# Optimization experiments

Hardware: AMD Instinct MI355X
Metric: run time of the kernel (lower is better)

Reference implementation:

```python
import jax, jax.numpy as jnp
import numpy as np
import math

B, N, D, K = 128, 2048, 256, 64


def setup_inputs() -> dict:
    key = jax.random.key(0)
    ks = jax.random.split(key, 8)
    latent = jax.random.normal(ks[0], (B, N, D), dtype=jnp.float32)
    token_mask = jax.random.uniform(ks[1], (B, N)) < 0.7
    token_mask = token_mask.at[:, 0].set(True)  # guarantee >=1 valid token per row
    scale = 1.0 / math.sqrt(D)
    Wq = jax.random.normal(ks[2], (D, D), dtype=jnp.float32) * scale
    bq = jax.random.normal(ks[3], (D,), dtype=jnp.float32) * 0.01
    Wk = jax.random.normal(ks[4], (D, D), dtype=jnp.float32) * scale
    bk = jax.random.normal(ks[5], (D,), dtype=jnp.float32) * 0.01
    Ws = jax.random.normal(ks[6], (D,), dtype=jnp.float32) * scale
    bs = jax.random.normal(ks[7], (1,), dtype=jnp.float32) * 0.01
    return {"latent": latent, "token_mask": token_mask, "Wq": Wq, "bq": bq,
            "Wk": Wk, "bk": bk, "Ws": Ws, "bs": bs}


def reference(latent, token_mask, Wq, bq, Wk, bk, Ws, bs):
    # latent: [B, N, D], token_mask: [B, N] bool
    d = latent.shape[-1]
    ego = latent[:, :1, :]                                   # [B, 1, D]
    query = jnp.einsum('bod,ed->boe', ego, Wq) + bq          # [B, 1, D]
    keys = jnp.einsum('bnd,ed->bne', latent, Wk) + bk        # [B, N, D]
    similarity = jnp.sum(query * keys, axis=-1) / jnp.sqrt(jnp.float32(d))  # [B, N]
    saliency = jnp.einsum('bnd,d->bn', latent, Ws) + bs[0]   # [B, N]
    scores = similarity + saliency
    scores = jnp.where(token_mask, scores, -jnp.inf)
    # force_ego = False -> no inf injection at slot 0
    selected_scores, selected_indices = jax.lax.top_k(scores, K)  # [B, K]
    # batched_index_select along token dim
    selected_tokens = jnp.take_along_axis(latent, selected_indices[:, :, None], axis=1)  # [B, K, D]
    sel_mask_f = jnp.take_along_axis(token_mask.astype(jnp.float32)[:, :, None],
                                     selected_indices[:, :, None], axis=1)[:, :, 0]
    selected_mask = sel_mask_f > 0.5                          # [B, K]
    # masked mean over token dim
    m = token_mask.astype(latent.dtype)
    global_latent = jnp.einsum('bnd,bn->bd', latent, m) / jnp.sum(m, axis=1, keepdims=True)  # [B, D]
    importance = jax.nn.softmax(jnp.where(selected_mask, selected_scores, -1e9), axis=1)     # [B, K]
    return selected_tokens, selected_mask, selected_indices, importance, global_latent
```

## Files before the change

### kernel.cpp

```cpp
#include <hip/hip_runtime.h>
#include <math.h>

#define B 128
#define N 2048
#define D 256
#define K 64
#define CH 16
#define RPC (N / CH)
#define MASKED_KEY 0x007FFFFFu

typedef unsigned long long u64;

#define OFF_V       0
#define OFF_C2      (OFF_V + B * D)
#define OFF_CNT     (OFF_C2 + B)
#define OFF_PART    (OFF_CNT + B)
#define OFF_MODE    (OFF_PART + B * CH * D)
#define OFF_LISTS   (OFF_MODE + 64)

#define O_TOK   0
#define O_MASK  (O_TOK + B * K * D)
#define O_IDX   (O_MASK + B * K)
#define O_IMP   (O_IDX + B * K)
#define O_GLOB  (O_IMP + B * K)

__device__ __forceinline__ bool mask_at(const void* p, int mode, int i) {
    if (mode == 1) return ((const unsigned char*)p)[i] != 0;
    if (mode == 2) return ((const float*)p)[i] != 0.0f;
    return ((const int*)p)[i] != 0;
}

__device__ __forceinline__ u64 wave_sort_desc(u64 P, int l) {
    #pragma unroll
    for (int k2 = 2; k2 <= 64; k2 <<= 1) {
        #pragma unroll
        for (int j = k2 >> 1; j >= 1; j >>= 1) {
            u64 o = __shfl_xor(P, j, 64);
            bool lower = (l & j) == 0;
            bool descB = (l & k2) == 0;
            bool og = o > P;
            if (og == (lower == descB)) P = o;
        }
    }
    return P;
}

__device__ __forceinline__ u64 wave_merge_desc(u64 P, int l) {
    #pragma unroll
    for (int j = 32; j >= 1; j >>= 1) {
        u64 o = __shfl_xor(P, j, 64);
        bool lower = (l & j) == 0;
        bool og = o > P;
        if (og == lower) P = o;
    }
    return P;
}

__global__ __launch_bounds__(256) void prep_kernel(
        const float* __restrict__ latent, const void* __restrict__ maskp,
        const float* __restrict__ Wq, const float* __restrict__ bq,
        const float* __restrict__ Wk, const float* __restrict__ bk,
        const float* __restrict__ Ws, const float* __restrict__ bs,
        float* __restrict__ v, float* __restrict__ c2, float* __restrict__ cnt,
        int* __restrict__ modep) {
    int b = blockIdx.x, t = threadIdx.x, w = t >> 6, l = t & 63;
    int g = l >> 4, i = l & 15;
    __shared__ float ego[D];
    __shared__ float q[D];
    __shared__ int smode;
    if (w == 0) {
        const unsigned int* mw = (const unsigned int*)maskp;
        bool isF = false, hasHigh = false;
        for (int k = 0; k < 16; ++k) {
            unsigned int x = mw[l * 16 + k];
            if (x == 0x3F800000u) isF = true;
            if (x & 0xFFFFFF00u) hasHigh = true;
        }
        unsigned long long bf = __ballot(isF);
        unsigned long long bh = __ballot(hasHigh);
        if (l == 0) smode = bf ? 2 : (bh ? 1 : 0);
    }
    ego[t] = latent[(size_t)b * N * D + t];
    __syncthreads();
    int mode = smode;
    if (b == 0 && t == 0) *modep = mode;

    const float4* e4 = (const float4*)ego;
    float4 ev0 = e4[i], ev1 = e4[i + 16], ev2 = e4[i + 32], ev3 = e4[i + 48];
    for (int it = 0; it < 16; ++it) {
        int r = w * 64 + it * 4 + g;
        const float4* row = (const float4*)(Wq + (size_t)r * D);
        float4 x0 = row[i], x1 = row[i + 16], x2 = row[i + 32], x3 = row[i + 48];
        float p = x0.x * ev0.x;
        p = fmaf(x0.y, ev0.y, p); p = fmaf(x0.z, ev0.z, p); p = fmaf(x0.w, ev0.w, p);
        p = fmaf(x1.x, ev1.x, p); p = fmaf(x1.y, ev1.y, p);
        p = fmaf(x1.z, ev1.z, p); p = fmaf(x1.w, ev1.w, p);
        p = fmaf(x2.x, ev2.x, p); p = fmaf(x2.y, ev2.y, p);
        p = fmaf(x2.z, ev2.z, p); p = fmaf(x2.w, ev2.w, p);
        p = fmaf(x3.x, ev3.x, p); p = fmaf(x3.y, ev3.y, p);
        p = fmaf(x3.z, ev3.z, p); p = fmaf(x3.w, ev3.w, p);
        #pragma unroll
        for (int m = 8; m >= 1; m >>= 1) p += __shfl_xor(p, m, 64);
        if (i == 0) q[r] = p + bq[r];
    }
    __syncthreads();

    float acc = 0.f;
    #pragma unroll 16
    for (int e = 0; e < D; ++e) acc = fmaf(q[e], Wk[(size_t)e * D + t], acc);
    v[b * D + t] = acc * 0.0625f + Ws[t];

    if (t < 64) {
        float p = 0.f;
        #pragma unroll
        for (int j = 0; j < 4; ++j) p = fmaf(q[t + 64 * j], bk[t + 64 * j], p);
        #pragma unroll
        for (int m = 32; m >= 1; m >>= 1) p += __shfl_xor(p, m, 64);
        if (t == 0) c2[b] = p * 0.0625f + bs[0];
    }
    int local = 0;
    for (int k = 0; k < N / D; ++k) local += mask_at(maskp, mode, b * N + t + D * k) ? 1 : 0;
    __shared__ int ctot;
    if (t == 0) ctot = 0;
    __syncthreads();
    atomicAdd(&ctot, local);
    __syncthreads();
    if (t == 0) cnt[b] = (float)ctot;
}

__global__ __launch_bounds__(256) void main_kernel(
        const float* __restrict__ latent, const void* __restrict__ maskp,
        const int* __restrict__ modep,
        const float* __restrict__ v, const float* __restrict__ c2,
        float* __restrict__ partials, u64* __restrict__ lists) {
    int b = blockIdx.y, ch = blockIdx.x;
    int t = threadIdx.x, w = t >> 6, l = t & 63;
    int g = l >> 4, i = l & 15;
    __shared__ float red[16][D];
    __shared__ u64 cand[RPC];
    __shared__ int rlds[RPC];
    __shared__ unsigned long long bal[2];
    __shared__ int s_M;

    int mode = *modep;
    int base = ch * RPC;
    if (t < RPC) cand[t] = ((u64)MASKED_KEY << 16);
    if (t < RPC) {
        bool m = mask_at(maskp, mode, b * N + base + t);
        unsigned long long bb = __ballot(m);
        if (l == 0) bal[t >> 6] = bb;
    }
    const float4* v4 = (const float4*)(v + b * D);
    float4 vv0 = v4[i], vv1 = v4[i + 16], vv2 = v4[i + 32], vv3 = v4[i + 48];
    float c2b = c2[b];
    __syncthreads();
    if (t < RPC) {
        unsigned long long bb = bal[t >> 6];
        bool m = (bb >> l) & 1ull;
        int off = ((t >> 6) ? (int)__popcll(bal[0]) : 0)
                + (int)__popcll(bb & ((1ull << l) - 1ull));
        if (m) rlds[off] = base + t;
    }
    if (t == 0) s_M = (int)(__popcll(bal[0]) + __popcll(bal[1]));
    float ax0=0,ay0=0,az0=0,aw0=0, ax1=0,ay1=0,az1=0,aw1=0;
    float ax2=0,ay2=0,az2=0,aw2=0, ax3=0,ay3=0,az3=0,aw3=0;
    const float4* lat4 = (const float4*)(latent + (size_t)b * N * D);
    __syncthreads();
    int M = s_M;

    #pragma unroll 2
    for (int jj = w * 4 + g; jj < M; jj += 16) {
        int n = rlds[jj];
        const float4* row = lat4 + (size_t)n * (D / 4);
        float4 x0 = row[i], x1 = row[i + 16], x2 = row[i + 32], x3 = row[i + 48];
        float p = x0.x * vv0.x;
        p = fmaf(x0.y, vv0.y, p); p = fmaf(x0.z, vv0.z, p); p = fmaf(x0.w, vv0.w, p);
        p = fmaf(x1.x, vv1.x, p); p = fmaf(x1.y, vv1.y, p);
        p = fmaf(x1.z, vv1.z, p); p = fmaf(x1.w, vv1.w, p);
        p = fmaf(x2.x, vv2.x, p); p = fmaf(x2.y, vv2.y, p);
        p = fmaf(x2.z, vv2.z, p); p = fmaf(x2.w, vv2.w, p);
        p = fmaf(x3.x, vv3.x, p); p = fmaf(x3.y, vv3.y, p);
        p = fmaf(x3.z, vv3.z, p); p = fmaf(x3.w, vv3.w, p);
        #pragma unroll
        for (int m = 8; m >= 1; m >>= 1) p += __shfl_xor(p, m, 64);
        if (i == 0) {
            unsigned int fu = __float_as_uint(p + c2b);
            unsigned int ky = (fu & 0x80000000u) ? ~fu : (fu | 0x80000000u);
            cand[jj] = ((u64)ky << 16) | (u64)(2047 - n);
        }
        ax0 += x0.x; ay0 += x0.y; az0 += x0.z; aw0 += x0.w;
        ax1 += x1.x; ay1 += x1.y; az1 += x1.z; aw1 += x1.w;
        ax2 += x2.x; ay2 += x2.y; az2 += x2.z; aw2 += x2.w;
        ax3 += x3.x; ay3 += x3.y; az3 += x3.z; aw3 += x3.w;
    }
    float* rr = red[w * 4 + g];
    rr[i*4+0]=ax0; rr[i*4+1]=ay0; rr[i*4+2]=az0; rr[i*4+3]=aw0;
    rr[64+i*4+0]=ax1; rr[64+i*4+1]=ay1; rr[64+i*4+2]=az1; rr[64+i*4+3]=aw1;
    rr[128+i*4+0]=ax2; rr[128+i*4+1]=ay2; rr[128+i*4+2]=az2; rr[128+i*4+3]=aw2;
    rr[192+i*4+0]=ax3; rr[192+i*4+1]=ay3; rr[192+i*4+2]=az3; rr[192+i*4+3]=aw3;
    __syncthreads();
    float s = 0.f;
    #pragma unroll
    for (int r = 0; r < 16; ++r) s += red[r][t];
    partials[((size_t)b * CH + ch) * D + t] = s;

    if (w == 0) {
        u64 A = wave_sort_desc(cand[l], l);
        u64 Bc = wave_sort_desc(cand[64 + l], l);
        u64 rev = __shfl_xor(Bc, 63, 64);
        A = (A > rev) ? A : rev;
        A = wave_merge_desc(A, l);
        lists[((size_t)b * CH + ch) * K + l] = A;
    }
}

__global__ __launch_bounds__(256) void epilogue_kernel(
        const u64* __restrict__ listsg, const float* __restrict__ latent,
        const float* __restrict__ partials, const float* __restrict__ cnt,
        float* __restrict__ out_mask, float* __restrict__ out_idx,
        float* __restrict__ out_imp, float* __restrict__ out_tok,
        float* __restrict__ out_glob) {
    int b = blockIdx.x, t = threadIdx.x, w = t >> 6, l = t & 63;
    __shared__ u64 lb[CH * K];
    __shared__ int sortedIdx[K];

    for (int q = 0; q < CH * K / 256; ++q)
        lb[t + 256 * q] = listsg[(size_t)b * CH * K + t + 256 * q];
    __syncthreads();

    if (w == 0) {
        u64 cur = lb[l];
        #pragma unroll
        for (int q = 1; q < CH; ++q) {
            u64 rev = lb[q * K + (63 - l)];
            cur = (cur > rev) ? cur : rev;
            cur = wave_merge_desc(cur, l);
        }
        unsigned int u = (unsigned int)(cur >> 16);
        int pos = 2047 - (int)(cur & 0xFFFFu);
        unsigned int fu = (u & 0x80000000u) ? (u ^ 0x80000000u) : ~u;
        float selv = __uint_as_float(fu);
        bool m = (u != MASKED_KEY);
        float x = m ? selv : -1e9f;
        float mx = x;
        #pragma unroll
        for (int mm = 1; mm <= 32; mm <<= 1) mx = fmaxf(mx, __shfl_xor(mx, mm, 64));
        float e = expf(x - mx);
        float sm = e;
        #pragma unroll
        for (int mm = 1; mm <= 32; mm <<= 1) sm += __shfl_xor(sm, mm, 64);
        out_idx[b * K + l] = (float)pos;
        out_mask[b * K + l] = m ? 1.f : 0.f;
        out_imp[b * K + l] = e / sm;
        sortedIdx[l] = pos;
    }
    __syncthreads();

    for (int r = w; r < K; r += 4) {
        int idx = sortedIdx[r];
        float4 x = ((const float4*)(latent + ((size_t)b * N + idx) * D))[l];
        ((float4*)(out_tok + ((size_t)b * K + r) * D))[l] = x;
    }
    float gs = 0.f;
    #pragma unroll
    for (int c = 0; c < CH; ++c) gs += partials[((size_t)b * CH + c) * D + t];
    out_glob[b * D + t] = gs / cnt[b];
}

extern "C" void kernel_launch(void* const* d_in, const int* in_sizes, int n_in,
                              void* d_out, int out_size, void* d_ws, size_t ws_size,
                              hipStream_t stream) {
    const float* latent = (const float*)d_in[0];
    const void*  maskp  = d_in[1];
    const float* Wq = (const float*)d_in[2];
    const float* bq = (const float*)d_in[3];
    const float* Wk = (const float*)d_in[4];
    const float* bk = (const float*)d_in[5];
    const float* Ws = (const float*)d_in[6];
    const float* bs = (const float*)d_in[7];

    float* ws = (float*)d_ws;
    float* v      = ws + OFF_V;
    float* c2     = ws + OFF_C2;
    float* cnt    = ws + OFF_CNT;
    float* part   = ws + OFF_PART;
    int*   modep  = (int*)(ws + OFF_MODE);
    u64*   lists  = (u64*)(ws + OFF_LISTS);
    float* out = (float*)d_out;

    hipLaunchKernelGGL(prep_kernel, dim3(B), dim3(256), 0, stream,
                       latent, maskp, Wq, bq, Wk, bk, Ws, bs, v, c2, cnt, modep);
    hipLaunchKernelGGL(main_kernel, dim3(CH, B), dim3(256), 0, stream,
                       latent, maskp, modep, v, c2, part, lists);
    hipLaunchKernelGGL(epilogue_kernel, dim3(B), dim3(256), 0, stream,
                       lists, latent, part, cnt,
                       out + O_MASK, out + O_IDX, out + O_IMP, out + O_TOK, out + O_GLOB);
}
```

Baseline: 72.53 us.

## Fuse prep, main and epilogue into one cooperative kernel with grid syncs

```diff
diff --git a/kernel.cpp b/kernel.cpp
--- a/kernel.cpp
+++ b/kernel.cpp
@@ -1,22 +1,25 @@
 #include <hip/hip_runtime.h>
+#include <hip/hip_cooperative_groups.h>
 #include <math.h>
+
+namespace cg = cooperative_groups;
 
 #define B 128
 #define N 2048
 #define D 256
 #define K 64
-#define CH 16
-#define RPC (N / CH)
+#define CHN 4
+#define RPW (N / CHN)
 #define MASKED_KEY 0x007FFFFFu
 
 typedef unsigned long long u64;
 
-#define OFF_V       0
+#define OFF_Q       0
+#define OFF_V       (OFF_Q + B * D)
 #define OFF_C2      (OFF_V + B * D)
 #define OFF_CNT     (OFF_C2 + B)
-#define OFF_PART    (OFF_CNT + B)
-#define OFF_MODE    (OFF_PART + B * CH * D)
-#define OFF_LISTS   (OFF_MODE + 64)
+#define OFF_PART    (OFF_CNT + B * CHN)
+#define OFF_LISTS   (OFF_PART + B * CHN * D)
 
 #define O_TOK   0
 #define O_MASK  (O_TOK + B * K * D)
@@ -56,18 +59,35 @@
     return P;
 }
 
-__global__ __launch_bounds__(256) void prep_kernel(
+__global__ __launch_bounds__(256, 2) void fused_kernel(
         const float* __restrict__ latent, const void* __restrict__ maskp,
         const float* __restrict__ Wq, const float* __restrict__ bq,
         const float* __restrict__ Wk, const float* __restrict__ bk,
         const float* __restrict__ Ws, const float* __restrict__ bs,
-        float* __restrict__ v, float* __restrict__ c2, float* __restrict__ cnt,
-        int* __restrict__ modep) {
-    int b = blockIdx.x, t = threadIdx.x, w = t >> 6, l = t & 63;
+        float* __restrict__ qbuf, float* __restrict__ v, float* __restrict__ c2,
+        int* __restrict__ cntpart, float* __restrict__ partials,
+        u64* __restrict__ lists,
+        float* __restrict__ out_mask, float* __restrict__ out_idx,
+        float* __restrict__ out_imp, float* __restrict__ out_tok,
+        float* __restrict__ out_glob) {
+    cg::grid_group grid = cg::this_grid();
+    int blk = blockIdx.x;
+    int b = blk >> 2, s = blk & 3;
+    int t = threadIdx.x, w = t >> 6, l = t & 63;
     int g = l >> 4, i = l & 15;
+
+    __shared__ float red[16][D];
+    __shared__ u64 cand[RPW];
+    __shared__ int rlds[RPW];
+    __shared__ u64 lb[CHN * K];
+    __shared__ int sortedIdx[K];
     __shared__ float ego[D];
-    __shared__ float q[D];
+    __shared__ float c2part[4];
     __shared__ int smode;
+    __shared__ unsigned long long bal[8];
+    __shared__ int s_M;
+    __shared__ float s_cnt;
+
     if (w == 0) {
         const unsigned int* mw = (const unsigned int*)maskp;
         bool isF = false, hasHigh = false;
@@ -83,85 +103,77 @@
     ego[t] = latent[(size_t)b * N * D + t];
     __syncthreads();
     int mode = smode;
-    if (b == 0 && t == 0) *modep = mode;
-
-    const float4* e4 = (const float4*)ego;
-    float4 ev0 = e4[i], ev1 = e4[i + 16], ev2 = e4[i + 32], ev3 = e4[i + 48];
-    for (int it = 0; it < 16; ++it) {
-        int r = w * 64 + it * 4 + g;
-        const float4* row = (const float4*)(Wq + (size_t)r * D);
-        float4 x0 = row[i], x1 = row[i + 16], x2 = row[i + 32], x3 = row[i + 48];
-        float p = x0.x * ev0.x;
-        p = fmaf(x0.y, ev0.y, p); p = fmaf(x0.z, ev0.z, p); p = fmaf(x0.w, ev0.w, p);
-        p = fmaf(x1.x, ev1.x, p); p = fmaf(x1.y, ev1.y, p);
-        p = fmaf(x1.z, ev1.z, p); p = fmaf(x1.w, ev1.w, p);
-        p = fmaf(x2.x, ev2.x, p); p = fmaf(x2.y, ev2.y, p);
-        p = fmaf(x2.z, ev2.z, p); p = fmaf(x2.w, ev2.w, p);
-        p = fmaf(x3.x, ev3.x, p); p = fmaf(x3.y, ev3.y, p);
-        p = fmaf(x3.z, ev3.z, p); p = fmaf(x3.w, ev3.w, p);
-        #pragma unroll
-        for (int m = 8; m >= 1; m >>= 1) p += __shfl_xor(p, m, 64);
-        if (i == 0) q[r] = p + bq[r];
-    }
-    __syncthreads();
-
-    float acc = 0.f;
-    #pragma unroll 16
-    for (int e = 0; e < D; ++e) acc = fmaf(q[e], Wk[(size_t)e * D + t], acc);
-    v[b * D + t] = acc * 0.0625f + Ws[t];
-
-    if (t < 64) {
-        float p = 0.f;
-        #pragma unroll
-        for (int j = 0; j < 4; ++j) p = fmaf(q[t + 64 * j], bk[t + 64 * j], p);
-        #pragma unroll
-        for (int m = 32; m >= 1; m >>= 1) p += __shfl_xor(p, m, 64);
-        if (t == 0) c2[b] = p * 0.0625f + bs[0];
-    }
-    int local = 0;
-    for (int k = 0; k < N / D; ++k) local += mask_at(maskp, mode, b * N + t + D * k) ? 1 : 0;
-    __shared__ int ctot;
-    if (t == 0) ctot = 0;
-    __syncthreads();
-    atomicAdd(&ctot, local);
-    __syncthreads();
-    if (t == 0) cnt[b] = (float)ctot;
-}
-
-__global__ __launch_bounds__(256) void main_kernel(
-        const float* __restrict__ latent, const void* __restrict__ maskp,
-        const int* __restrict__ modep,
-        const float* __restrict__ v, const float* __restrict__ c2,
-        float* __restrict__ partials, u64* __restrict__ lists) {
-    int b = blockIdx.y, ch = blockIdx.x;
-    int t = threadIdx.x, w = t >> 6, l = t & 63;
-    int g = l >> 4, i = l & 15;
-    __shared__ float red[16][D];
-    __shared__ u64 cand[RPC];
-    __shared__ int rlds[RPC];
-    __shared__ unsigned long long bal[2];
-    __shared__ int s_M;
-
-    int mode = *modep;
-    int base = ch * RPC;
-    if (t < RPC) cand[t] = ((u64)MASKED_KEY << 16);
-    if (t < RPC) {
-        bool m = mask_at(maskp, mode, b * N + base + t);
-        unsigned long long bb = __ballot(m);
-        if (l == 0) bal[t >> 6] = bb;
+
+    {
+        const float4* e4 = (const float4*)ego;
+        float4 ev0 = e4[i], ev1 = e4[i + 16], ev2 = e4[i + 32], ev3 = e4[i + 48];
+        #pragma unroll
+        for (int it = 0; it < 4; ++it) {
+            int r = s * 64 + w * 16 + it * 4 + g;
+            const float4* row = (const float4*)(Wq + (size_t)r * D);
+            float4 x0 = row[i], x1 = row[i + 16], x2 = row[i + 32], x3 = row[i + 48];
+            float p = x0.x * ev0.x;
+            p = fmaf(x0.y, ev0.y, p); p = fmaf(x0.z, ev0.z, p); p = fmaf(x0.w, ev0.w, p);
+            p = fmaf(x1.x, ev1.x, p); p = fmaf(x1.y, ev1.y, p);
+            p = fmaf(x1.z, ev1.z, p); p = fmaf(x1.w, ev1.w, p);
+            p = fmaf(x2.x, ev2.x, p); p = fmaf(x2.y, ev2.y, p);
+            p = fmaf(x2.z, ev2.z, p); p = fmaf(x2.w, ev2.w, p);
+            p = fmaf(x3.x, ev3.x, p); p = fmaf(x3.y, ev3.y, p);
+            p = fmaf(x3.z, ev3.z, p); p = fmaf(x3.w, ev3.w, p);
+            #pragma unroll
+            for (int m = 8; m >= 1; m >>= 1) p += __shfl_xor(p, m, 64);
+            if (i == 0) qbuf[b * D + r] = p + bq[r];
+        }
+    }
+    grid.sync();
+
+    {
+        float (*redB)[64] = (float(*)[64])red;
+        int c = s * 64 + (t & 63);
+        int e0 = (t >> 6) * 64;
+        float part = 0.f;
+        #pragma unroll 16
+        for (int e = e0; e < e0 + 64; ++e)
+            part = fmaf(qbuf[b * D + e], Wk[(size_t)e * D + c], part);
+        redB[t >> 6][t & 63] = part;
+        if (s == 0) {
+            float pc = qbuf[b * D + t] * bk[t];
+            #pragma unroll
+            for (int m = 32; m >= 1; m >>= 1) pc += __shfl_xor(pc, m, 64);
+            if (l == 0) c2part[w] = pc;
+        }
+        __syncthreads();
+        if (t < 64) {
+            float sv = redB[0][t] + redB[1][t] + redB[2][t] + redB[3][t];
+            v[b * D + s * 64 + t] = sv * 0.0625f + Ws[s * 64 + t];
+        }
+        if (s == 0 && t == 0)
+            c2[b] = (c2part[0] + c2part[1] + c2part[2] + c2part[3]) * 0.0625f + bs[0];
+    }
+    grid.sync();
+
+    int base = s * RPW;
+    bool m0, m1;
+    {
+        m0 = mask_at(maskp, mode, b * N + base + t);
+        m1 = mask_at(maskp, mode, b * N + base + 256 + t);
+        unsigned long long b0 = __ballot(m0);
+        unsigned long long b1 = __ballot(m1);
+        if (l == 0) { bal[w] = b0; bal[4 + w] = b1; }
+        cand[t] = ((u64)MASKED_KEY << 16);
+        cand[256 + t] = ((u64)MASKED_KEY << 16);
+        __syncthreads();
+        int pre[8];
+        int run = 0;
+        #pragma unroll
+        for (int q2 = 0; q2 < 8; ++q2) { pre[q2] = run; run += (int)__popcll(bal[q2]); }
+        if (m0) rlds[pre[w] + (int)__popcll(bal[w] & ((1ull << l) - 1ull))] = base + t;
+        if (m1) rlds[pre[4 + w] + (int)__popcll(bal[4 + w] & ((1ull << l) - 1ull))] = base + 256 + t;
+        if (t == 0) { s_M = run; cntpart[b * CHN + s] = run; }
     }
     const float4* v4 = (const float4*)(v + b * D);
     float4 vv0 = v4[i], vv1 = v4[i + 16], vv2 = v4[i + 32], vv3 = v4[i + 48];
     float c2b = c2[b];
-    __syncthreads();
-    if (t < RPC) {
-        unsigned long long bb = bal[t >> 6];
-        bool m = (bb >> l) & 1ull;
-        int off = ((t >> 6) ? (int)__popcll(bal[0]) : 0)
-                + (int)__popcll(bb & ((1ull << l) - 1ull));
-        if (m) rlds[off] = base + t;
-    }
-    if (t == 0) s_M = (int)(__popcll(bal[0]) + __popcll(bal[1]));
     float ax0=0,ay0=0,az0=0,aw0=0, ax1=0,ay1=0,az1=0,aw1=0;
     float ax2=0,ay2=0,az2=0,aw2=0, ax3=0,ay3=0,az3=0,aw3=0;
     const float4* lat4 = (const float4*)(latent + (size_t)b * N * D);
@@ -193,78 +205,88 @@
         ax2 += x2.x; ay2 += x2.y; az2 += x2.z; aw2 += x2.w;
         ax3 += x3.x; ay3 += x3.y; az3 += x3.z; aw3 += x3.w;
     }
-    float* rr = red[w * 4 + g];
-    rr[i*4+0]=ax0; rr[i*4+1]=ay0; rr[i*4+2]=az0; rr[i*4+3]=aw0;
-    rr[64+i*4+0]=ax1; rr[64+i*4+1]=ay1; rr[64+i*4+2]=az1; rr[64+i*4+3]=aw1;
-    rr[128+i*4+0]=ax2; rr[128+i*4+1]=ay2; rr[128+i*4+2]=az2; rr[128+i*4+3]=aw2;
-    rr[192+i*4+0]=ax3; rr[192+i*4+1]=ay3; rr[192+i*4+2]=az3; rr[192+i*4+3]=aw3;
-    __syncthreads();
-    float s = 0.f;
-    #pragma unroll
-    for (int r = 0; r < 16; ++r) s += red[r][t];
-    partials[((size_t)b * CH + ch) * D + t] = s;
-
+    {
+        float* rr = red[w * 4 + g];
+        rr[i*4+0]=ax0; rr[i*4+1]=ay0; rr[i*4+2]=az0; rr[i*4+3]=aw0;
+        rr[64+i*4+0]=ax1; rr[64+i*4+1]=ay1; rr[64+i*4+2]=az1; rr[64+i*4+3]=aw1;
+        rr[128+i*4+0]=ax2; rr[128+i*4+1]=ay2; rr[128+i*4+2]=az2; rr[128+i*4+3]=aw2;
+        rr[192+i*4+0]=ax3; rr[192+i*4+1]=ay3; rr[192+i*4+2]=az3; rr[192+i*4+3]=aw3;
+        __syncthreads();
+        float sm = 0.f;
+        #pragma unroll
+        for (int r = 0; r < 16; ++r) sm += red[r][t];
+        partials[((size_t)b * CHN + s) * D + t] = sm;
+    }
     if (w == 0) {
         u64 A = wave_sort_desc(cand[l], l);
-        u64 Bc = wave_sort_desc(cand[64 + l], l);
-        u64 rev = __shfl_xor(Bc, 63, 64);
-        A = (A > rev) ? A : rev;
-        A = wave_merge_desc(A, l);
-        lists[((size_t)b * CH + ch) * K + l] = A;
-    }
-}
-
-__global__ __launch_bounds__(256) void epilogue_kernel(
-        const u64* __restrict__ listsg, const float* __restrict__ latent,
-        const float* __restrict__ partials, const float* __restrict__ cnt,
-        float* __restrict__ out_mask, float* __restrict__ out_idx,
-        float* __restrict__ out_imp, float* __restrict__ out_tok,
-        float* __restrict__ out_glob) {
-    int b = blockIdx.x, t = threadIdx.x, w = t >> 6, l = t & 63;
-    __shared__ u64 lb[CH * K];
-    __shared__ int sortedIdx[K];
-
-    for (int q = 0; q < CH * K / 256; ++q)
-        lb[t + 256 * q] = listsg[(size_t)b * CH * K + t + 256 * q];
+        #pragma unroll
+        for (int q = 1; q < 8; ++q) {
+            u64 Bc = wave_sort_desc(cand[q * 64 + l], l);
+            u64 rev = __shfl_xor(Bc, 63, 64);
+            A = (A > rev) ? A : rev;
+            A = wave_merge_desc(A, l);
+        }
+        lists[((size_t)b * CHN + s) * K + l] = A;
+    }
+    grid.sync();
+
+    if (t < CHN * K) lb[t] = lists[(size_t)b * CHN * K + t];
+    if (t == 0) {
+        int ct = 0;
+        #pragma unroll
+        for (int q = 0; q < CHN; ++q) ct += cntpart[b * CHN + q];
+        s_cnt = (float)ct;
+    }
     __syncthreads();
 
     if (w == 0) {
         u64 cur = lb[l];
         #pragma unroll
-        for (int q = 1; q < CH; ++q) {
+        for (int q = 1; q < CHN; ++q) {
             u64 rev = lb[q * K + (63 - l)];
             cur = (cur > rev) ? cur : rev;
             cur = wave_merge_desc(cur, l);
         }
         unsigned int u = (unsigned int)(cur >> 16);
         int pos = 2047 - (int)(cur & 0xFFFFu);
-        unsigned int fu = (u & 0x80000000u) ? (u ^ 0x80000000u) : ~u;
-        float selv = __uint_as_float(fu);
-        bool m = (u != MASKED_KEY);
-        float x = m ? selv : -1e9f;
-        float mx = x;
-        #pragma unroll
-        for (int mm = 1; mm <= 32; mm <<= 1) mx = fmaxf(mx, __shfl_xor(mx, mm, 64));
-        float e = expf(x - mx);
-        float sm = e;
-        #pragma unroll
-        for (int mm = 1; mm <= 32; mm <<= 1) sm += __shfl_xor(sm, mm, 64);
-        out_idx[b * K + l] = (float)pos;
-        out_mask[b * K + l] = m ? 1.f : 0.f;
-        out_imp[b * K + l] = e / sm;
         sortedIdx[l] = pos;
+        if (s == 0) {
+            unsigned int fu = (u & 0x80000000u) ? (u ^ 0x80000000u) : ~u;
+            float selv = __uint_as_float(fu);
+            bool m = (u != MASKED_KEY);
+            float x = m ? selv : -1e9f;
+            float mx = x;
+            #pragma unroll
+            for (int mm = 1; mm <= 32; mm <<= 1) mx = fmaxf(mx, __shfl_xor(mx, mm, 64));
+            float e = expf(x - mx);
+            float sm = e;
+            #pragma unroll
+            for (int mm = 1; mm <= 32; mm <<= 1) sm += __shfl_xor(sm, mm, 64);
+            out_idx[b * K + l] = (float)pos;
+            out_mask[b * K + l] = m ? 1.f : 0.f;
+            out_imp[b * K + l] = e / sm;
+        }
     }
     __syncthreads();
 
-    for (int r = w; r < K; r += 4) {
+    #pragma unroll
+    for (int rr2 = 0; rr2 < 4; ++rr2) {
+        int r = s * 16 + w * 4 + rr2;
         int idx = sortedIdx[r];
         float4 x = ((const float4*)(latent + ((size_t)b * N + idx) * D))[l];
         ((float4*)(out_tok + ((size_t)b * K + r) * D))[l] = x;
     }
-    float gs = 0.f;
-    #pragma unroll
-    for (int c = 0; c < CH; ++c) gs += partials[((size_t)b * CH + c) * D + t];
-    out_glob[b * D + t] = gs / cnt[b];
+    {
+        float (*redB)[64] = (float(*)[64])red;
+        float pv = partials[((size_t)b * CHN + (t >> 6)) * D + s * 64 + (t & 63)];
+        __syncthreads();
+        redB[t >> 6][t & 63] = pv;
+        __syncthreads();
+        if (t < 64) {
+            float sv = redB[0][t] + redB[1][t] + redB[2][t] + redB[3][t];
+            out_glob[b * D + s * 64 + t] = sv / s_cnt;
+        }
+    }
 }
 
 extern "C" void kernel_launch(void* const* d_in, const int* in_sizes, int n_in,
@@ -280,19 +302,25 @@
     const float* bs = (const float*)d_in[7];
 
     float* ws = (float*)d_ws;
+    float* qbuf   = ws + OFF_Q;
     float* v      = ws + OFF_V;
     float* c2     = ws + OFF_C2;
-    float* cnt    = ws + OFF_CNT;
+    int*   cntp   = (int*)(ws + OFF_CNT);
     float* part   = ws + OFF_PART;
-    int*   modep  = (int*)(ws + OFF_MODE);
     u64*   lists  = (u64*)(ws + OFF_LISTS);
     float* out = (float*)d_out;
-
-    hipLaunchKernelGGL(prep_kernel, dim3(B), dim3(256), 0, stream,
-                       latent, maskp, Wq, bq, Wk, bk, Ws, bs, v, c2, cnt, modep);
-    hipLaunchKernelGGL(main_kernel, dim3(CH, B), dim3(256), 0, stream,
-                       latent, maskp, modep, v, c2, part, lists);
-    hipLaunchKernelGGL(epilogue_kernel, dim3(B), dim3(256), 0, stream,
-                       lists, latent, part, cnt,
-                       out + O_MASK, out + O_IDX, out + O_IMP, out + O_TOK, out + O_GLOB);
-}
+    float* om = out + O_MASK;
+    float* oi = out + O_IDX;
+    float* oim = out + O_IMP;
+    float* ot = out + O_TOK;
+    float* og = out + O_GLOB;
+
+    void* args[] = {
+        (void*)&latent, (void*)&maskp, (void*)&Wq, (void*)&bq, (void*)&Wk,
+        (void*)&bk, (void*)&Ws, (void*)&bs, (void*)&qbuf, (void*)&v,
+        (void*)&c2, (void*)&cntp, (void*)&part, (void*)&lists,
+        (void*)&om, (void*)&oi, (void*)&oim, (void*)&ot, (void*)&og
+    };
+    hipLaunchCooperativeKernel((const void*)fused_kernel, dim3(B * CHN), dim3(256),
+                               args, 0, stream);
+}
```

New measurement: 200.6 us. 177% more time.

## Split prep and epilogue kernels across more blocks per batch row

Applied to the files above, without the earlier changes.

```diff
diff --git a/kernel.cpp b/kernel.cpp
--- a/kernel.cpp
+++ b/kernel.cpp
@@ -63,10 +63,13 @@
         const float* __restrict__ Ws, const float* __restrict__ bs,
         float* __restrict__ v, float* __restrict__ c2, float* __restrict__ cnt,
         int* __restrict__ modep) {
-    int b = blockIdx.x, t = threadIdx.x, w = t >> 6, l = t & 63;
+    int blk = blockIdx.x;
+    int b = blk >> 1, s = blk & 1;
+    int t = threadIdx.x, w = t >> 6, l = t & 63;
     int g = l >> 4, i = l & 15;
     __shared__ float ego[D];
     __shared__ float q[D];
+    __shared__ float redp[2][128];
     __shared__ int smode;
     if (w == 0) {
         const unsigned int* mw = (const unsigned int*)maskp;
@@ -83,7 +86,7 @@
     ego[t] = latent[(size_t)b * N * D + t];
     __syncthreads();
     int mode = smode;
-    if (b == 0 && t == 0) *modep = mode;
+    if (blk == 0 && t == 0) *modep = mode;
 
     const float4* e4 = (const float4*)ego;
     float4 ev0 = e4[i], ev1 = e4[i + 16], ev2 = e4[i + 32], ev3 = e4[i + 48];
@@ -105,27 +108,38 @@
     }
     __syncthreads();
 
-    float acc = 0.f;
-    #pragma unroll 16
-    for (int e = 0; e < D; ++e) acc = fmaf(q[e], Wk[(size_t)e * D + t], acc);
-    v[b * D + t] = acc * 0.0625f + Ws[t];
-
-    if (t < 64) {
-        float p = 0.f;
-        #pragma unroll
-        for (int j = 0; j < 4; ++j) p = fmaf(q[t + 64 * j], bk[t + 64 * j], p);
-        #pragma unroll
-        for (int m = 32; m >= 1; m >>= 1) p += __shfl_xor(p, m, 64);
-        if (t == 0) c2[b] = p * 0.0625f + bs[0];
-    }
-    int local = 0;
-    for (int k = 0; k < N / D; ++k) local += mask_at(maskp, mode, b * N + t + D * k) ? 1 : 0;
-    __shared__ int ctot;
-    if (t == 0) ctot = 0;
-    __syncthreads();
-    atomicAdd(&ctot, local);
-    __syncthreads();
-    if (t == 0) cnt[b] = (float)ctot;
+    {
+        int c = s * 128 + (t & 127);
+        int eh = t >> 7;
+        float acc = 0.f;
+        #pragma unroll 16
+        for (int e = eh * 128; e < eh * 128 + 128; ++e)
+            acc = fmaf(q[e], Wk[(size_t)e * D + c], acc);
+        redp[eh][t & 127] = acc;
+    }
+    if (s == 0) {
+        if (t < 64) {
+            float p = 0.f;
+            #pragma unroll
+            for (int j = 0; j < 4; ++j) p = fmaf(q[t + 64 * j], bk[t + 64 * j], p);
+            #pragma unroll
+            for (int m = 32; m >= 1; m >>= 1) p += __shfl_xor(p, m, 64);
+            if (t == 0) c2[b] = p * 0.0625f + bs[0];
+        }
+    } else {
+        int local = 0;
+        for (int k = 0; k < N / D; ++k) local += mask_at(maskp, mode, b * N + t + D * k) ? 1 : 0;
+        __shared__ int ctot;
+        if (t == 0) ctot = 0;
+        __syncthreads();
+        atomicAdd(&ctot, local);
+        __syncthreads();
+        if (t == 0) cnt[b] = (float)ctot;
+        __syncthreads();
+    }
+    __syncthreads();
+    if (t < 128)
+        v[b * D + s * 128 + t] = (redp[0][t] + redp[1][t]) * 0.0625f + Ws[s * 128 + t];
 }
 
 __global__ __launch_bounds__(256) void main_kernel(
@@ -220,51 +234,79 @@
         float* __restrict__ out_mask, float* __restrict__ out_idx,
         float* __restrict__ out_imp, float* __restrict__ out_tok,
         float* __restrict__ out_glob) {
-    int b = blockIdx.x, t = threadIdx.x, w = t >> 6, l = t & 63;
+    int blk = blockIdx.x;
+    int b = blk >> 2, s = blk & 3;
+    int t = threadIdx.x, w = t >> 6, l = t & 63;
     __shared__ u64 lb[CH * K];
+    __shared__ u64 wres[4][K];
     __shared__ int sortedIdx[K];
+    __shared__ float redc[4][64];
 
     for (int q = 0; q < CH * K / 256; ++q)
         lb[t + 256 * q] = listsg[(size_t)b * CH * K + t + 256 * q];
     __syncthreads();
 
-    if (w == 0) {
-        u64 cur = lb[l];
-        #pragma unroll
-        for (int q = 1; q < CH; ++q) {
-            u64 rev = lb[q * K + (63 - l)];
+    {
+        u64 cur = lb[(w * 4) * K + l];
+        #pragma unroll
+        for (int q = 1; q < 4; ++q) {
+            u64 rev = lb[(w * 4 + q) * K + (63 - l)];
             cur = (cur > rev) ? cur : rev;
             cur = wave_merge_desc(cur, l);
         }
+        wres[w][l] = cur;
+    }
+    __syncthreads();
+    if (w == 0) {
+        u64 cur = wres[0][l];
+        #pragma unroll
+        for (int q = 1; q < 4; ++q) {
+            u64 rev = wres[q][63 - l];
+            cur = (cur > rev) ? cur : rev;
+            cur = wave_merge_desc(cur, l);
+        }
         unsigned int u = (unsigned int)(cur >> 16);
         int pos = 2047 - (int)(cur & 0xFFFFu);
-        unsigned int fu = (u & 0x80000000u) ? (u ^ 0x80000000u) : ~u;
-        float selv = __uint_as_float(fu);
-        bool m = (u != MASKED_KEY);
-        float x = m ? selv : -1e9f;
-        float mx = x;
-        #pragma unroll
-        for (int mm = 1; mm <= 32; mm <<= 1) mx = fmaxf(mx, __shfl_xor(mx, mm, 64));
-        float e = expf(x - mx);
-        float sm = e;
-        #pragma unroll
-        for (int mm = 1; mm <= 32; mm <<= 1) sm += __shfl_xor(sm, mm, 64);
-        out_idx[b * K + l] = (float)pos;
-        out_mask[b * K + l] = m ? 1.f : 0.f;
-        out_imp[b * K + l] = e / sm;
         sortedIdx[l] = pos;
-    }
-    __syncthreads();
-
-    for (int r = w; r < K; r += 4) {
+        if (s == 0) {
+            unsigned int fu = (u & 0x80000000u) ? (u ^ 0x80000000u) : ~u;
+            float selv = __uint_as_float(fu);
+            bool m = (u != MASKED_KEY);
+            float x = m ? selv : -1e9f;
+            float mx = x;
+            #pragma unroll
+            for (int mm = 1; mm <= 32; mm <<= 1) mx = fmaxf(mx, __shfl_xor(mx, mm, 64));
+            float e = expf(x - mx);
+            float sm = e;
+            #pragma unroll
+            for (int mm = 1; mm <= 32; mm <<= 1) sm += __shfl_xor(sm, mm, 64);
+            out_idx[b * K + l] = (float)pos;
+            out_mask[b * K + l] = m ? 1.f : 0.f;
+            out_imp[b * K + l] = e / sm;
+        }
+    }
+    __syncthreads();
+
+    #pragma unroll
+    for (int rr2 = 0; rr2 < 4; ++rr2) {
+        int r = s * 16 + w * 4 + rr2;
         int idx = sortedIdx[r];
         float4 x = ((const float4*)(latent + ((size_t)b * N + idx) * D))[l];
         ((float4*)(out_tok + ((size_t)b * K + r) * D))[l] = x;
     }
-    float gs = 0.f;
-    #pragma unroll
-    for (int c = 0; c < CH; ++c) gs += partials[((size_t)b * CH + c) * D + t];
-    out_glob[b * D + t] = gs / cnt[b];
+    {
+        int c = s * 64 + (t & 63);
+        int qd = t >> 6;
+        float gs = 0.f;
+        #pragma unroll
+        for (int q = 0; q < 4; ++q)
+            gs += partials[((size_t)b * CH + qd * 4 + q) * D + c];
+        redc[qd][t & 63] = gs;
+        __syncthreads();
+        if (t < 64)
+            out_glob[b * D + s * 64 + t] =
+                (redc[0][t] + redc[1][t] + redc[2][t] + redc[3][t]) / cnt[b];
+    }
 }
 
 extern "C" void kernel_launch(void* const* d_in, const int* in_sizes, int n_in,
@@ -288,11 +330,11 @@
     u64*   lists  = (u64*)(ws + OFF_LISTS);
     float* out = (float*)d_out;
 
-    hipLaunchKernelGGL(prep_kernel, dim3(B), dim3(256), 0, stream,
+    hipLaunchKernelGGL(prep_kernel, dim3(B * 2), dim3(256), 0, stream,
                        latent, maskp, Wq, bq, Wk, bk, Ws, bs, v, c2, cnt, modep);
     hipLaunchKernelGGL(main_kernel, dim3(CH, B), dim3(256), 0, stream,
                        latent, maskp, modep, v, c2, part, lists);
-    hipLaunchKernelGGL(epilogue_kernel, dim3(B), dim3(256), 0, stream,
+    hipLaunchKernelGGL(epilogue_kernel, dim3(B * 4), dim3(256), 0, stream,
                        lists, latent, part, cnt,
                        out + O_MASK, out + O_IDX, out + O_IMP, out + O_TOK, out + O_GLOB);
 }
```

New measurement: 61.55 us. 1.18x faster.
